# Optimization experiments

Hardware: AMD Instinct MI355X
Metric: run time of the kernel (lower is better)

Reference implementation:

```python
import jax, jax.numpy as jnp
import numpy as np

B = 65536
STATE_DIM = 96
ACTION_DIM = 32
IN_FEATURES = STATE_DIM + ACTION_DIM  # 128
HIDDEN = 256
NUM_HEADS = 200
OUT_FEATURES = 1


def setup_inputs() -> dict:
    key = jax.random.key(0)
    ks = jax.random.split(key, 9)
    state = jax.random.normal(ks[0], (B, STATE_DIM), dtype=jnp.float32)
    action = jax.random.normal(ks[1], (B, ACTION_DIM), dtype=jnp.float32)
    alphas = jax.random.uniform(ks[2], (NUM_HEADS,), dtype=jnp.float32)
    W1 = jax.random.normal(ks[3], (HIDDEN, IN_FEATURES), dtype=jnp.float32) * 0.05
    b1 = jax.random.normal(ks[4], (HIDDEN,), dtype=jnp.float32) * 0.05
    W2 = jax.random.normal(ks[5], (HIDDEN, HIDDEN), dtype=jnp.float32) * 0.05
    b2 = jax.random.normal(ks[6], (HIDDEN,), dtype=jnp.float32) * 0.05
    # stacked head params: heads[h] is Linear(256 -> out_features)
    Wh = jax.random.normal(ks[7], (NUM_HEADS, OUT_FEATURES, HIDDEN), dtype=jnp.float32) * 0.05
    bh = jax.random.normal(ks[8], (NUM_HEADS, OUT_FEATURES), dtype=jnp.float32) * 0.05
    return {"state": state, "action": action, "alphas": alphas,
            "W1": W1, "b1": b1, "W2": W2, "b2": b2, "Wh": Wh, "bh": bh}


def reference(state, action, alphas, W1, b1, W2, b2, Wh, bh):
    x = jnp.concatenate([state, action], axis=1)          # [B, 128]
    x = jax.nn.relu(x @ W1.T + b1)                         # [B, 256]
    x = jax.nn.relu(x @ W2.T + b2)                         # [B, 256]
    # sum_h alpha_h * (x @ Wh[h].T + bh[h])  ==  x @ (sum_h alpha_h Wh[h]).T + sum_h alpha_h bh[h]
    Wc = jnp.einsum('h,hod->od', alphas, Wh)               # [out, 256]
    bc = jnp.einsum('h,ho->o', alphas, bh)                 # [out]
    return x @ Wc.T + bc                                   # [B, out]
```

## Files before the change

### kernel.cpp

```cpp
#include <hip/hip_runtime.h>
#include <hip/hip_bf16.h>


#define B_TOTAL 65536
#define SDIM 96
#define ADIM 32
#define IN_F 128
#define HID 256
#define NHEADS 200
#define BM 64
#define NTILES 4
#define XS_PITCH 132
#define H1_PITCH 260

typedef __bf16 bf16;
typedef __attribute__((ext_vector_type(4))) __bf16 bf16x4;
typedef __attribute__((ext_vector_type(8))) __bf16 bf16x8;
typedef __attribute__((ext_vector_type(4))) float f32x4;

static __device__ __forceinline__ float4 pack_bf16x8_as_f4(float4 a, float4 b) {
    union { bf16x8 h; float4 f; } u;
    u.h = (bf16x8){(bf16)a.x, (bf16)a.y, (bf16)a.z, (bf16)a.w,
                   (bf16)b.x, (bf16)b.y, (bf16)b.z, (bf16)b.w};
    return u.f;
}
static __device__ __forceinline__ bf16x8 as_bf16x8(float4 v) {
    union { float4 f; bf16x8 h; } u;
    u.f = v;
    return u.h;
}
static __device__ __forceinline__ void pin_f4(float4& v) {
    asm volatile("" : "+v"(v.x), "+v"(v.y), "+v"(v.z), "+v"(v.w));
}

__global__ __launch_bounds__(512, 2) void critic_kernel(
        const float* __restrict__ state, const float* __restrict__ action,
        const float* __restrict__ alphas,
        const float* __restrict__ W1, const float* __restrict__ b1,
        const float* __restrict__ W2, const float* __restrict__ b2,
        const float* __restrict__ Wh, const float* __restrict__ bh,
        float* __restrict__ out) {

    __shared__ bf16  xs[BM * XS_PITCH];
    __shared__ bf16  h1s[BM * H1_PITCH];
    __shared__ float sPart[8][BM];
    __shared__ float sWcP[2][HID];
    __shared__ float sWc[HID + 1];

    const int tid  = threadIdx.x;
    const int wave = tid >> 6;
    const int lane = tid & 63;
    const int q    = lane >> 4;
    const int ln   = lane & 15;
    const int colw = wave * 32;
    const int brow0 = blockIdx.x * (BM * NTILES);

    float4 w1s[4][2];
    #pragma unroll
    for (int ks = 0; ks < 4; ++ks)
        #pragma unroll
        for (int nt = 0; nt < 2; ++nt) {
            const float* p = W1 + (size_t)(colw + nt * 16 + ln) * IN_F + ks * 32 + q * 8;
            w1s[ks][nt] = pack_bf16x8_as_f4(((const float4*)p)[0], ((const float4*)p)[1]);
        }

    float4 w2s[8][2];
    #pragma unroll
    for (int ks = 0; ks < 8; ++ks)
        #pragma unroll
        for (int nt = 0; nt < 2; ++nt) {
            const float* p = W2 + (size_t)(colw + nt * 16 + ln) * HID + ks * 32 + q * 8;
            w2s[ks][nt] = pack_bf16x8_as_f4(((const float4*)p)[0], ((const float4*)p)[1]);
        }

    #pragma unroll
    for (int ks = 0; ks < 4; ++ks)
        #pragma unroll
        for (int nt = 0; nt < 2; ++nt)
            pin_f4(w1s[ks][nt]);
    #pragma unroll
    for (int ks = 0; ks < 8; ++ks)
        #pragma unroll
        for (int nt = 0; nt < 2; ++nt)
            pin_f4(w2s[ks][nt]);

    f32x4 b1v[2], b2v[2];
    #pragma unroll
    for (int nt = 0; nt < 2; ++nt) {
        const int n4 = colw + nt * 16 + q * 4;
        b1v[nt] = *(const f32x4*)&b1[n4];
        b2v[nt] = *(const f32x4*)&b2[n4];
    }

    {
        const int c    = tid & 255;
        const int half = tid >> 8;
        float p = 0.f;
        #pragma unroll 10
        for (int i = 0; i < 100; ++i) {
            const int h = half * 100 + i;
            p += alphas[h] * Wh[(size_t)h * HID + c];
        }
        sWcP[half][c] = p;
    }
    if (tid < 64) {
        float p = 0.f;
        #pragma unroll
        for (int i = 0; i < 4; ++i) {
            const int h = tid + i * 64;
            if (h < NHEADS) p += alphas[h] * bh[h];
        }
        #pragma unroll
        for (int off = 1; off < 64; off <<= 1)
            p += __shfl_xor(p, off, 64);
        if (tid == 0) sWc[HID] = p;
    }

    const int c0r  = tid >> 4;
    const int c0c8 = tid & 15;
    const int c1r  = (tid + 512) >> 4;
    const int c1c8 = (tid + 512) & 15;

    float4 px[2][2];
    {
        const float* s0 = (c0c8 < 12) ? (state  + (size_t)(brow0 + c0r) * SDIM + c0c8 * 8)
                                      : (action + (size_t)(brow0 + c0r) * ADIM + (c0c8 - 12) * 8);
        const float* s1 = (c1c8 < 12) ? (state  + (size_t)(brow0 + c1r) * SDIM + c1c8 * 8)
                                      : (action + (size_t)(brow0 + c1r) * ADIM + (c1c8 - 12) * 8);
        px[0][0] = ((const float4*)s0)[0]; px[0][1] = ((const float4*)s0)[1];
        px[1][0] = ((const float4*)s1)[0]; px[1][1] = ((const float4*)s1)[1];
    }

    for (int t = 0; t < NTILES; ++t) {
        const int row0 = brow0 + t * BM;

        *(bf16x8*)&xs[c0r * XS_PITCH + c0c8 * 8] =
            (bf16x8){(bf16)px[0][0].x, (bf16)px[0][0].y, (bf16)px[0][0].z, (bf16)px[0][0].w,
                     (bf16)px[0][1].x, (bf16)px[0][1].y, (bf16)px[0][1].z, (bf16)px[0][1].w};
        *(bf16x8*)&xs[c1r * XS_PITCH + c1c8 * 8] =
            (bf16x8){(bf16)px[1][0].x, (bf16)px[1][0].y, (bf16)px[1][0].z, (bf16)px[1][0].w,
                     (bf16)px[1][1].x, (bf16)px[1][1].y, (bf16)px[1][1].z, (bf16)px[1][1].w};
        __syncthreads();

        if (t == 0 && tid < HID)
            sWc[tid] = sWcP[0][tid] + sWcP[1][tid];

        if (t + 1 < NTILES) {
            const int n0 = row0 + BM;
            const float* s0 = (c0c8 < 12) ? (state  + (size_t)(n0 + c0r) * SDIM + c0c8 * 8)
                                          : (action + (size_t)(n0 + c0r) * ADIM + (c0c8 - 12) * 8);
            const float* s1 = (c1c8 < 12) ? (state  + (size_t)(n0 + c1r) * SDIM + c1c8 * 8)
                                          : (action + (size_t)(n0 + c1r) * ADIM + (c1c8 - 12) * 8);
            px[0][0] = ((const float4*)s0)[0]; px[0][1] = ((const float4*)s0)[1];
            px[1][0] = ((const float4*)s1)[0]; px[1][1] = ((const float4*)s1)[1];
        }

        f32x4 acc[4][2];
        #pragma unroll
        for (int mt = 0; mt < 4; ++mt)
            #pragma unroll
            for (int nt = 0; nt < 2; ++nt)
                acc[mt][nt] = (f32x4){0.f, 0.f, 0.f, 0.f};

        #pragma unroll
        for (int ks = 0; ks < 4; ++ks) {
            const int k0 = ks * 32 + q * 8;
            bf16x8 bfr[4];
            #pragma unroll
            for (int mt = 0; mt < 4; ++mt)
                bfr[mt] = *(const bf16x8*)&xs[(mt * 16 + ln) * XS_PITCH + k0];
            #pragma unroll
            for (int mt = 0; mt < 4; ++mt)
                #pragma unroll
                for (int nt = 0; nt < 2; ++nt)
                    acc[mt][nt] = __builtin_amdgcn_mfma_f32_16x16x32_bf16(
                        as_bf16x8(w1s[ks][nt]), bfr[mt], acc[mt][nt], 0, 0, 0);
        }
        #pragma unroll
        for (int nt = 0; nt < 2; ++nt)
            #pragma unroll
            for (int mt = 0; mt < 4; ++mt) {
                bf16x4 v4;
                #pragma unroll
                for (int r = 0; r < 4; ++r) {
                    float v = acc[mt][nt][r] + b1v[nt][r];
                    v = v > 0.f ? v : 0.f;
                    v4[r] = (bf16)v;
                }
                *(bf16x4*)&h1s[(mt * 16 + ln) * H1_PITCH + colw + nt * 16 + q * 4] = v4;
            }
        __syncthreads();

        #pragma unroll
        for (int mt = 0; mt < 4; ++mt)
            #pragma unroll
            for (int nt = 0; nt < 2; ++nt)
                acc[mt][nt] = (f32x4){0.f, 0.f, 0.f, 0.f};

        #pragma unroll
        for (int ks = 0; ks < 8; ++ks) {
            const int k0 = ks * 32 + q * 8;
            bf16x8 bfr[4];
            #pragma unroll
            for (int mt = 0; mt < 4; ++mt)
                bfr[mt] = *(const bf16x8*)&h1s[(mt * 16 + ln) * H1_PITCH + k0];
            #pragma unroll
            for (int mt = 0; mt < 4; ++mt)
                #pragma unroll
                for (int nt = 0; nt < 2; ++nt)
                    acc[mt][nt] = __builtin_amdgcn_mfma_f32_16x16x32_bf16(
                        as_bf16x8(w2s[ks][nt]), bfr[mt], acc[mt][nt], 0, 0, 0);
        }

        f32x4 wcv[2];
        #pragma unroll
        for (int nt = 0; nt < 2; ++nt)
            wcv[nt] = *(const f32x4*)&sWc[colw + nt * 16 + q * 4];

        float partial[4];
        #pragma unroll
        for (int mt = 0; mt < 4; ++mt) {
            float p = 0.f;
            #pragma unroll
            for (int nt = 0; nt < 2; ++nt)
                #pragma unroll
                for (int r = 0; r < 4; ++r) {
                    float v = acc[mt][nt][r] + b2v[nt][r];
                    v = v > 0.f ? v : 0.f;
                    p += v * wcv[nt][r];
                }
            partial[mt] = p;
        }
        #pragma unroll
        for (int mt = 0; mt < 4; ++mt) {
            partial[mt] += __shfl_xor(partial[mt], 16, 64);
            partial[mt] += __shfl_xor(partial[mt], 32, 64);
        }
        if (q == 0) {
            #pragma unroll
            for (int mt = 0; mt < 4; ++mt)
                sPart[wave][mt * 16 + ln] = partial[mt];
        }
        __syncthreads();

        if (tid < BM) {
            float v = sWc[HID];
            #pragma unroll
            for (int w = 0; w < 8; ++w) v += sPart[w][tid];
            out[row0 + tid] = v;
        }
    }
}

extern "C" void kernel_launch(void* const* d_in, const int* in_sizes, int n_in,
                              void* d_out, int out_size, void* d_ws, size_t ws_size,
                              hipStream_t stream) {
    const float* state  = (const float*)d_in[0];
    const float* action = (const float*)d_in[1];
    const float* alphas = (const float*)d_in[2];
    const float* W1     = (const float*)d_in[3];
    const float* b1     = (const float*)d_in[4];
    const float* W2     = (const float*)d_in[5];
    const float* b2     = (const float*)d_in[6];
    const float* Wh     = (const float*)d_in[7];
    const float* bh     = (const float*)d_in[8];
    float* out = (float*)d_out;

    critic_kernel<<<B_TOTAL / (BM * NTILES), 512, 0, stream>>>(
        state, action, alphas, W1, b1, W2, b2, Wh, bh, out);
}
```

Before: 112.5 us.

## Double the row tile to 128 and move next-tile prefetch after layer 1

Each block now processes two 128-row tiles instead of four 64-row tiles, so each wave issues more MFMAs per shared-memory phase and there are half as many barriers per block. Shared memory moves to dynamic allocation (about 100 KB), set through hipFuncSetAttribute. The next tile's input prefetch moves to after the first GEMM's barrier. The larger accumulators (64 floats) and the px buffers (32 floats) on top of the register-resident weights risk spills under launch_bounds(512,2). The larger LDS footprint may also cut occupancy to one block per CU.

New measurement: 157.0 us. 39.5% more time.

```diff
diff --git a/kernel.cpp b/kernel.cpp
--- a/kernel.cpp
+++ b/kernel.cpp
@@ -8,10 +8,16 @@
 #define IN_F 128
 #define HID 256
 #define NHEADS 200
-#define BM 64
-#define NTILES 4
+#define BM 128
+#define NTILES 2
 #define XS_PITCH 132
 #define H1_PITCH 260
+#define XS_BYTES (BM * XS_PITCH * 2)
+#define H1_BYTES (BM * H1_PITCH * 2)
+#define SP_BYTES (8 * BM * 4)
+#define WCP_BYTES (2 * HID * 4)
+#define WC_BYTES ((HID + 1) * 4)
+#define SMEM_BYTES (XS_BYTES + H1_BYTES + SP_BYTES + WCP_BYTES + WC_BYTES)
 
 typedef __bf16 bf16;
 typedef __attribute__((ext_vector_type(4))) __bf16 bf16x4;
@@ -41,11 +47,12 @@
         const float* __restrict__ Wh, const float* __restrict__ bh,
         float* __restrict__ out) {
 
-    __shared__ bf16  xs[BM * XS_PITCH];
-    __shared__ bf16  h1s[BM * H1_PITCH];
-    __shared__ float sPart[8][BM];
-    __shared__ float sWcP[2][HID];
-    __shared__ float sWc[HID + 1];
+    extern __shared__ char smem[];
+    bf16*  xs    = (bf16*)smem;
+    bf16*  h1s   = (bf16*)(smem + XS_BYTES);
+    float* sPart = (float*)(smem + XS_BYTES + H1_BYTES);
+    float* sWcP  = (float*)(smem + XS_BYTES + H1_BYTES + SP_BYTES);
+    float* sWc   = (float*)(smem + XS_BYTES + H1_BYTES + SP_BYTES + WCP_BYTES);
 
     const int tid  = threadIdx.x;
     const int wave = tid >> 6;
@@ -63,7 +70,6 @@
             const float* p = W1 + (size_t)(colw + nt * 16 + ln) * IN_F + ks * 32 + q * 8;
             w1s[ks][nt] = pack_bf16x8_as_f4(((const float4*)p)[0], ((const float4*)p)[1]);
         }
-
     float4 w2s[8][2];
     #pragma unroll
     for (int ks = 0; ks < 8; ++ks)
@@ -72,7 +78,6 @@
             const float* p = W2 + (size_t)(colw + nt * 16 + ln) * HID + ks * 32 + q * 8;
             w2s[ks][nt] = pack_bf16x8_as_f4(((const float4*)p)[0], ((const float4*)p)[1]);
         }
-
     #pragma unroll
     for (int ks = 0; ks < 4; ++ks)
         #pragma unroll
@@ -101,7 +106,7 @@
             const int h = half * 100 + i;
             p += alphas[h] * Wh[(size_t)h * HID + c];
         }
-        sWcP[half][c] = p;
+        sWcP[half * HID + c] = p;
     }
     if (tid < 64) {
         float p = 0.f;
@@ -116,48 +121,38 @@
         if (tid == 0) sWc[HID] = p;
     }
 
-    const int c0r  = tid >> 4;
-    const int c0c8 = tid & 15;
-    const int c1r  = (tid + 512) >> 4;
-    const int c1c8 = (tid + 512) & 15;
-
-    float4 px[2][2];
-    {
-        const float* s0 = (c0c8 < 12) ? (state  + (size_t)(brow0 + c0r) * SDIM + c0c8 * 8)
-                                      : (action + (size_t)(brow0 + c0r) * ADIM + (c0c8 - 12) * 8);
-        const float* s1 = (c1c8 < 12) ? (state  + (size_t)(brow0 + c1r) * SDIM + c1c8 * 8)
-                                      : (action + (size_t)(brow0 + c1r) * ADIM + (c1c8 - 12) * 8);
-        px[0][0] = ((const float4*)s0)[0]; px[0][1] = ((const float4*)s0)[1];
-        px[1][0] = ((const float4*)s1)[0]; px[1][1] = ((const float4*)s1)[1];
+    float4 px[4][2];
+    #pragma unroll
+    for (int i = 0; i < 4; ++i) {
+        const int c  = tid + i * 512;
+        const int r  = c >> 4;
+        const int c8 = c & 15;
+        const float* s = (c8 < 12) ? (state  + (size_t)(brow0 + r) * SDIM + c8 * 8)
+                                   : (action + (size_t)(brow0 + r) * ADIM + (c8 - 12) * 8);
+        px[i][0] = ((const float4*)s)[0];
+        px[i][1] = ((const float4*)s)[1];
     }
 
     for (int t = 0; t < NTILES; ++t) {
         const int row0 = brow0 + t * BM;
 
-        *(bf16x8*)&xs[c0r * XS_PITCH + c0c8 * 8] =
-            (bf16x8){(bf16)px[0][0].x, (bf16)px[0][0].y, (bf16)px[0][0].z, (bf16)px[0][0].w,
-                     (bf16)px[0][1].x, (bf16)px[0][1].y, (bf16)px[0][1].z, (bf16)px[0][1].w};
-        *(bf16x8*)&xs[c1r * XS_PITCH + c1c8 * 8] =
-            (bf16x8){(bf16)px[1][0].x, (bf16)px[1][0].y, (bf16)px[1][0].z, (bf16)px[1][0].w,
-                     (bf16)px[1][1].x, (bf16)px[1][1].y, (bf16)px[1][1].z, (bf16)px[1][1].w};
+        #pragma unroll
+        for (int i = 0; i < 4; ++i) {
+            const int c  = tid + i * 512;
+            const int r  = c >> 4;
+            const int c8 = c & 15;
+            *(bf16x8*)&xs[r * XS_PITCH + c8 * 8] =
+                (bf16x8){(bf16)px[i][0].x, (bf16)px[i][0].y, (bf16)px[i][0].z, (bf16)px[i][0].w,
+                         (bf16)px[i][1].x, (bf16)px[i][1].y, (bf16)px[i][1].z, (bf16)px[i][1].w};
+        }
         __syncthreads();
 
         if (t == 0 && tid < HID)
-            sWc[tid] = sWcP[0][tid] + sWcP[1][tid];
-
-        if (t + 1 < NTILES) {
-            const int n0 = row0 + BM;
-            const float* s0 = (c0c8 < 12) ? (state  + (size_t)(n0 + c0r) * SDIM + c0c8 * 8)
-                                          : (action + (size_t)(n0 + c0r) * ADIM + (c0c8 - 12) * 8);
-            const float* s1 = (c1c8 < 12) ? (state  + (size_t)(n0 + c1r) * SDIM + c1c8 * 8)
-                                          : (action + (size_t)(n0 + c1r) * ADIM + (c1c8 - 12) * 8);
-            px[0][0] = ((const float4*)s0)[0]; px[0][1] = ((const float4*)s0)[1];
-            px[1][0] = ((const float4*)s1)[0]; px[1][1] = ((const float4*)s1)[1];
-        }
-
-        f32x4 acc[4][2];
-        #pragma unroll
-        for (int mt = 0; mt < 4; ++mt)
+            sWc[tid] = sWcP[tid] + sWcP[HID + tid];
+
+        f32x4 acc[8][2];
+        #pragma unroll
+        for (int mt = 0; mt < 8; ++mt)
             #pragma unroll
             for (int nt = 0; nt < 2; ++nt)
                 acc[mt][nt] = (f32x4){0.f, 0.f, 0.f, 0.f};
@@ -165,12 +160,12 @@
         #pragma unroll
         for (int ks = 0; ks < 4; ++ks) {
             const int k0 = ks * 32 + q * 8;
-            bf16x8 bfr[4];
-            #pragma unroll
-            for (int mt = 0; mt < 4; ++mt)
+            bf16x8 bfr[8];
+            #pragma unroll
+            for (int mt = 0; mt < 8; ++mt)
                 bfr[mt] = *(const bf16x8*)&xs[(mt * 16 + ln) * XS_PITCH + k0];
             #pragma unroll
-            for (int mt = 0; mt < 4; ++mt)
+            for (int mt = 0; mt < 8; ++mt)
                 #pragma unroll
                 for (int nt = 0; nt < 2; ++nt)
                     acc[mt][nt] = __builtin_amdgcn_mfma_f32_16x16x32_bf16(
@@ -179,7 +174,7 @@
         #pragma unroll
         for (int nt = 0; nt < 2; ++nt)
             #pragma unroll
-            for (int mt = 0; mt < 4; ++mt) {
+            for (int mt = 0; mt < 8; ++mt) {
                 bf16x4 v4;
                 #pragma unroll
                 for (int r = 0; r < 4; ++r) {
@@ -191,8 +186,22 @@
             }
         __syncthreads();
 
-        #pragma unroll
-        for (int mt = 0; mt < 4; ++mt)
+        if (t + 1 < NTILES) {
+            const int n0 = brow0 + (t + 1) * BM;
+            #pragma unroll
+            for (int i = 0; i < 4; ++i) {
+                const int c  = tid + i * 512;
+                const int r  = c >> 4;
+                const int c8 = c & 15;
+                const float* s = (c8 < 12) ? (state  + (size_t)(n0 + r) * SDIM + c8 * 8)
+                                           : (action + (size_t)(n0 + r) * ADIM + (c8 - 12) * 8);
+                px[i][0] = ((const float4*)s)[0];
+                px[i][1] = ((const float4*)s)[1];
+            }
+        }
+
+        #pragma unroll
+        for (int mt = 0; mt < 8; ++mt)
             #pragma unroll
             for (int nt = 0; nt < 2; ++nt)
                 acc[mt][nt] = (f32x4){0.f, 0.f, 0.f, 0.f};
@@ -200,12 +209,12 @@
         #pragma unroll
         for (int ks = 0; ks < 8; ++ks) {
             const int k0 = ks * 32 + q * 8;
-            bf16x8 bfr[4];
-            #pragma unroll
-            for (int mt = 0; mt < 4; ++mt)
+            bf16x8 bfr[8];
+            #pragma unroll
+            for (int mt = 0; mt < 8; ++mt)
                 bfr[mt] = *(const bf16x8*)&h1s[(mt * 16 + ln) * H1_PITCH + k0];
             #pragma unroll
-            for (int mt = 0; mt < 4; ++mt)
+            for (int mt = 0; mt < 8; ++mt)
                 #pragma unroll
                 for (int nt = 0; nt < 2; ++nt)
                     acc[mt][nt] = __builtin_amdgcn_mfma_f32_16x16x32_bf16(
@@ -217,9 +226,9 @@
         for (int nt = 0; nt < 2; ++nt)
             wcv[nt] = *(const f32x4*)&sWc[colw + nt * 16 + q * 4];
 
-        float partial[4];
-        #pragma unroll
-        for (int mt = 0; mt < 4; ++mt) {
+        float partial[8];
+        #pragma unroll
+        for (int mt = 0; mt < 8; ++mt) {
             float p = 0.f;
             #pragma unroll
             for (int nt = 0; nt < 2; ++nt)
@@ -232,21 +241,21 @@
             partial[mt] = p;
         }
         #pragma unroll
-        for (int mt = 0; mt < 4; ++mt) {
+        for (int mt = 0; mt < 8; ++mt) {
             partial[mt] += __shfl_xor(partial[mt], 16, 64);
             partial[mt] += __shfl_xor(partial[mt], 32, 64);
         }
         if (q == 0) {
             #pragma unroll
-            for (int mt = 0; mt < 4; ++mt)
-                sPart[wave][mt * 16 + ln] = partial[mt];
+            for (int mt = 0; mt < 8; ++mt)
+                sPart[wave * BM + mt * 16 + ln] = partial[mt];
         }
         __syncthreads();
 
         if (tid < BM) {
             float v = sWc[HID];
             #pragma unroll
-            for (int w = 0; w < 8; ++w) v += sPart[w][tid];
+            for (int w = 0; w < 8; ++w) v += sPart[w * BM + tid];
             out[row0 + tid] = v;
         }
     }
@@ -266,6 +275,10 @@
     const float* bh     = (const float*)d_in[8];
     float* out = (float*)d_out;
 
-    critic_kernel<<<B_TOTAL / (BM * NTILES), 512, 0, stream>>>(
+    (void)hipFuncSetAttribute((const void*)critic_kernel,
+                              hipFuncAttributeMaxDynamicSharedMemorySize,
+                              SMEM_BYTES);
+
+    critic_kernel<<<B_TOTAL / (BM * NTILES), 512, SMEM_BYTES, stream>>>(
         state, action, alphas, W1, b1, W2, b2, Wh, bh, out);
 }
```
